# Kernel optimization log

Hardware: AMD Instinct MI355X
Metric: run time of the kernel (lower is better)

The kernel has to match this reference:

```python
import jax, jax.numpy as jnp
import numpy as np

N_CELLS = 6
N_OPS = 5
HIDDEN = 1024
IN_DIM = 376
OUT_DIM = 17
MAX_OUTPUT = 1.0
TAU = 1.0
BATCH = 2048

# op order matches the torch module: Tanh, ReLU, ELU, LeakyReLU(0.01), NullOp
ACTS = [jnp.tanh, jax.nn.relu, jax.nn.elu,
        lambda v: jax.nn.leaky_relu(v, 0.01),
        lambda v: jnp.zeros_like(v)]


def _apply_ops(pre):
    # pre: [j, o, b, h] -> apply the o-th activation to the o-th slice
    return jnp.stack([ACTS[o](pre[:, o]) for o in range(N_OPS)], axis=1)


def setup_inputs() -> dict:
    key = jax.random.key(0)
    ks = jax.random.split(key, 8)
    bw0 = 1.0 / np.sqrt(IN_DIM)
    bwh = 1.0 / np.sqrt(HIDDEN)
    x = jax.random.normal(ks[0], (BATCH, IN_DIM), dtype=jnp.float32)
    # stacked edge weights: W0 for cell-0 edges (input_dim -> hidden),
    # Wh[i-1] for cell-i edges (hidden -> hidden), i = 1..n_cells-2
    W0 = jax.random.uniform(ks[1], (N_CELLS, N_OPS, IN_DIM, HIDDEN), minval=-bw0, maxval=bw0, dtype=jnp.float32)
    b0 = jax.random.uniform(ks[2], (N_CELLS, N_OPS, HIDDEN), minval=-bw0, maxval=bw0, dtype=jnp.float32)
    Wh = jax.random.uniform(ks[3], (N_CELLS - 2, N_CELLS, N_OPS, HIDDEN, HIDDEN), minval=-bwh, maxval=bwh, dtype=jnp.float32)
    bh = jax.random.uniform(ks[4], (N_CELLS - 2, N_CELLS, N_OPS, HIDDEN), minval=-bwh, maxval=bwh, dtype=jnp.float32)
    Wout = jax.random.uniform(ks[5], (HIDDEN, OUT_DIM), minval=-bwh, maxval=bwh, dtype=jnp.float32)
    bout = jax.random.uniform(ks[6], (OUT_DIM,), minval=-bwh, maxval=bwh, dtype=jnp.float32)
    log_alphas = jnp.full((N_CELLS - 1, N_CELLS, N_OPS), -np.log(N_OPS), dtype=jnp.float32)
    # Gumbel noise (the torch module draws this in self.sample())
    u = jax.random.uniform(ks[7], (N_CELLS - 1, N_CELLS, N_OPS), minval=1e-6, maxval=1.0 - 1e-6, dtype=jnp.float32)
    eps = -jnp.log(-jnp.log(u))
    return {"x": x, "W0": W0, "b0": b0, "Wh": Wh, "bh": bh,
            "Wout": Wout, "bout": bout, "log_alphas": log_alphas, "eps": eps}


def reference(x, W0, b0, Wh, bh, Wout, bout, log_alphas, eps):
    # Gumbel-softmax mixing weights over the op axis
    z = jax.nn.softmax((log_alphas + eps) / TAU, axis=-1)  # [n_cells-1, n_cells, n_ops]
    # cell 0 feeds every node j >= 1: one batched GEMM over (j, o)
    pre0 = jnp.einsum('bd,jodh->jobh', x, W0[1:]) + b0[1:, :, None, :]
    outs = [(1, _apply_ops(pre0))]  # (first absolute j index, [j, o, b, h])
    tmp = None
    for i in range(1, N_CELLS):
        # node i input: weighted sum over all incoming edges k < i and ops o
        acc = jnp.zeros((x.shape[0], HIDDEN), dtype=x.dtype)
        for k in range(i):
            start, arr = outs[k]
            acc = acc + jnp.einsum('o,obh->bh', z[k, i], arr[i - start])
        if i < N_CELLS - 1:
            # node i feeds nodes j > i: batched GEMM over (j, o)
            pre = jnp.einsum('bh,johg->jobg', acc, Wh[i - 1, i + 1:]) + bh[i - 1, i + 1:, :, None, :]
            outs.append((i + 1, _apply_ops(pre)))
        tmp = acc
    return MAX_OUTPUT * jnp.tanh(tmp @ Wout + bout)
```

## Files before the change

### kernel.cpp

```cpp
#include <hip/hip_runtime.h>
#include <hip/hip_fp16.h>

typedef unsigned short u16;
typedef _Float16 f16;
typedef __attribute__((ext_vector_type(4))) u16 u16x4;
typedef __attribute__((ext_vector_type(8))) f16 f16x8;
typedef __attribute__((ext_vector_type(4))) float f32x4;

#define BATCH   2048
#define IN_DIM  376
#define KPAD0   384
#define HIDDEN  1024
#define OUT_DIM 17

#define WS_Z     0
#define WS_X16   1024
#define WS_ACC16 (WS_X16 + (size_t)BATCH*KPAD0*2)
#define WS_ACCF  (WS_ACC16 + (size_t)4*BATCH*HIDDEN*2)
#define WS_W0T   (WS_ACCF + (size_t)5*BATCH*HIDDEN*4)
#define WS_WHT   (WS_W0T + (size_t)20*HIDDEN*KPAD0*2)

__device__ __constant__ int D_PREF[5] = {0, 0, 4, 7, 9};

__device__ inline void gll16(const void* g, void* l) {
    __builtin_amdgcn_global_load_lds(
        (const __attribute__((address_space(1))) unsigned int*)g,
        (__attribute__((address_space(3))) unsigned int*)l, 16, 0, 0);
}

__global__ void z_kernel(const float* __restrict__ la, const float* __restrict__ ep,
                         float* __restrict__ z) {
    int t = threadIdx.x;
    if (t >= 30) return;
    float v[5]; float mx = -1e30f;
    #pragma unroll
    for (int o = 0; o < 5; ++o) { v[o] = la[t*5+o] + ep[t*5+o]; mx = fmaxf(mx, v[o]); }
    float s = 0.f;
    #pragma unroll
    for (int o = 0; o < 5; ++o) { v[o] = expf(v[o] - mx); s += v[o]; }
    float inv = 1.f / s;
    #pragma unroll
    for (int o = 0; o < 5; ++o) z[t*5+o] = v[o] * inv;
}

__global__ void xcvt_kernel(const float* __restrict__ x, u16* __restrict__ x16) {
    int idx = blockIdx.x * 256 + threadIdx.x;
    int b = idx / KPAD0, c = idx % KPAD0;
    float v = (c < IN_DIM) ? x[(size_t)b*IN_DIM + c] : 0.f;
    f16 h = (f16)v;
    x16[idx] = __builtin_bit_cast(u16, h);
}

__global__ void wtrans0_kernel(const float* __restrict__ W0, u16* __restrict__ dst) {
    __shared__ u16 sT[64*68];
    int bid = blockIdx.x;
    int mat = bid / 96, rem = bid % 96;
    int kt = rem / 16, nt = rem % 16;
    int i = mat / 4 + 1, o = mat % 4;
    const float* src = W0 + (size_t)(i*5 + o) * IN_DIM * HIDDEN;
    int t = threadIdx.x;
    #pragma unroll
    for (int p = 0; p < 16; ++p) {
        int e = p*256 + t;
        int kr = e >> 6, nc = e & 63;
        int k = kt*64 + kr;
        float v = (k < IN_DIM) ? src[(size_t)k*HIDDEN + nt*64 + nc] : 0.f;
        f16 h = (f16)v;
        sT[nc*68 + kr] = __builtin_bit_cast(u16, h);
    }
    __syncthreads();
    u16* d = dst + (size_t)mat * HIDDEN * KPAD0;
    #pragma unroll
    for (int p = 0; p < 4; ++p) {
        int c = p*256 + t;
        int nc = c >> 4, k4 = (c & 15) * 4;
        u16x4 v;
        #pragma unroll
        for (int j = 0; j < 4; ++j) v[j] = sT[nc*68 + k4 + j];
        *(u16x4*)&d[(size_t)(nt*64 + nc)*KPAD0 + kt*64 + k4] = v;
    }
}

__global__ void wtransH_kernel(const float* __restrict__ Wh, u16* __restrict__ dst) {
    const int SK[10] = {1,1,1,1,2,2,2,3,3,4};
    const int SI[10] = {2,3,4,5,3,4,5,4,5,5};
    __shared__ u16 sT[64*68];
    int bid = blockIdx.x;
    int mat = bid >> 8, rem = bid & 255;
    int kt = rem / 16, nt = rem % 16;
    int e = mat / 4, o = mat % 4;
    const float* src = Wh + (size_t)(((SK[e]-1)*6 + SI[e])*5 + o) * HIDDEN * HIDDEN;
    int t = threadIdx.x;
    #pragma unroll
    for (int p = 0; p < 16; ++p) {
        int ee = p*256 + t;
        int kr = ee >> 6, nc = ee & 63;
        float v = src[(size_t)(kt*64 + kr)*HIDDEN + nt*64 + nc];
        f16 h = (f16)v;
        sT[nc*68 + kr] = __builtin_bit_cast(u16, h);
    }
    __syncthreads();
    u16* d = dst + (size_t)mat * HIDDEN * HIDDEN;
    #pragma unroll
    for (int p = 0; p < 4; ++p) {
        int c = p*256 + t;
        int nc = c >> 4, k4 = (c & 15) * 4;
        u16x4 v;
        #pragma unroll
        for (int j = 0; j < 4; ++j) v[j] = sT[nc*68 + k4 + j];
        *(u16x4*)&d[(size_t)(nt*64 + nc)*HIDDEN + kt*64 + k4] = v;
    }
}

__global__ void zero_kernel(float* __restrict__ p) {
    int idx = blockIdx.x * 256 + threadIdx.x;
    *(f32x4*)&p[(size_t)idx*4] = (f32x4){0.f, 0.f, 0.f, 0.f};
}

__global__ void cvt_kernel(const float* __restrict__ src, u16* __restrict__ dst) {
    int idx = blockIdx.x * 256 + threadIdx.x;
    f32x4 v = *(const f32x4*)&src[(size_t)idx*4];
    u16x4 h;
    #pragma unroll
    for (int j = 0; j < 4; ++j) { f16 x = (f16)v[j]; h[j] = __builtin_bit_cast(u16, x); }
    *(u16x4*)&dst[(size_t)idx*4] = h;
}

__global__ __launch_bounds__(256)
void step_kernel(int stepi,
                 const u16* __restrict__ x16, const u16* __restrict__ acc16,
                 float* __restrict__ accf,
                 const u16* __restrict__ w0t, const u16* __restrict__ wht,
                 const float* __restrict__ b0, const float* __restrict__ bh,
                 const float* __restrict__ zws) {
    __shared__ alignas(16) u16 sA[64*64];
    __shared__ alignas(16) u16 sB[4][64*64];
    const int t = threadIdx.x;
    const int lane = t & 63, wid = t >> 6;
    const int l15 = lane & 15, lk = lane >> 4;

    const int bid  = blockIdx.x;
    const int slot = bid & 7;
    const int q    = bid >> 3;
    const int m0   = (q & 31) * 64;
    const int e    = (q >> 5) * 8 + slot;
    const int k    = e >> 4;
    const int n0   = (e & 15) * 64;

    const u16* Ap; int ldA, nks;
    const u16* Wt; int ldW;
    const float* bias;
    if (k == 0) {
        Ap = x16; ldA = KPAD0; nks = KPAD0/64;
        Wt = w0t + (size_t)((stepi-1)*4) * HIDDEN * KPAD0; ldW = KPAD0;
        bias = b0 + (size_t)(stepi*5) * HIDDEN;
    } else {
        Ap = acc16 + (size_t)(k-1) * BATCH * HIDDEN; ldA = HIDDEN; nks = HIDDEN/64;
        int eidx = D_PREF[k] + (stepi - k - 1);
        Wt = wht + (size_t)(eidx*4) * HIDDEN * HIDDEN; ldW = HIDDEN;
        bias = bh + (size_t)(((k-1)*6 + stepi)*5) * HIDDEN;
    }
    const float* zp = zws + (k*6 + stepi)*5;

    const int srow = lane >> 3;
    const int sc   = (lane & 7) ^ srow;

    const u16* aG0 = Ap + (size_t)(m0 + wid*16 + srow)     * ldA + sc*8;
    const u16* aG1 = Ap + (size_t)(m0 + wid*16 + 8 + srow) * ldA + sc*8;
    u16* aL0 = &sA[(wid*2)   * 512];
    u16* aL1 = &sA[(wid*2+1) * 512];
    const u16* Wop = Wt + (size_t)wid * HIDDEN * ldW;
    const u16* bG[8];
    #pragma unroll
    for (int p = 0; p < 8; ++p)
        bG[p] = Wop + (size_t)(n0 + p*8 + srow) * ldW + sc*8;
    u16* bL = &sB[wid][0];

    f32x4 acc[4][4] = {};

    for (int kb = 0; kb < nks; ++kb) {
        const int koff = kb * 64;
        gll16(aG0 + koff, aL0);
        gll16(aG1 + koff, aL1);
        #pragma unroll
        for (int p = 0; p < 8; ++p)
            gll16(bG[p] + koff, bL + p*512);
        __syncthreads();
        #pragma unroll
        for (int kc = 0; kc < 2; ++kc) {
            f16x8 af[4], bf[4];
            #pragma unroll
            for (int f = 0; f < 4; ++f) {
                int row = f*16 + l15;
                int cc = (kc*4 + lk) ^ (row & 7);
                af[f] = *(const f16x8*)&sA[row*64 + cc*8];
            }
            #pragma unroll
            for (int o = 0; o < 4; ++o) {
                int row = wid*16 + l15;
                int cc = (kc*4 + lk) ^ (row & 7);
                bf[o] = *(const f16x8*)&sB[o][row*64 + cc*8];
            }
            #pragma unroll
            for (int o = 0; o < 4; ++o)
                #pragma unroll
                for (int f = 0; f < 4; ++f)
                    acc[f][o] = __builtin_amdgcn_mfma_f32_16x16x32_f16(af[f], bf[o], acc[f][o], 0, 0, 0);
        }
        __syncthreads();
    }

    const int colw = n0 + wid*16 + l15;
    float outv[4][4] = {};
    #pragma unroll
    for (int o = 0; o < 4; ++o) {
        float zv = zp[o];
        float bv = bias[(size_t)o*HIDDEN + colw];
        #pragma unroll
        for (int f = 0; f < 4; ++f)
            #pragma unroll
            for (int r = 0; r < 4; ++r) {
                float pre = acc[f][o][r] + bv;
                float a;
                if      (o == 0) a = tanhf(pre);
                else if (o == 1) a = fmaxf(pre, 0.f);
                else if (o == 2) a = (pre > 0.f) ? pre : expm1f(pre);
                else             a = (pre > 0.f) ? pre : 0.01f * pre;
                outv[f][r] += zv * a;
            }
    }
    #pragma unroll
    for (int f = 0; f < 4; ++f)
        #pragma unroll
        for (int r = 0; r < 4; ++r)
            atomicAdd(&accf[(size_t)(m0 + f*16 + lk*4 + r)*HIDDEN + colw], outv[f][r]);
}

__global__ void out_kernel(const float* __restrict__ acc5, const float* __restrict__ Wout,
                           const float* __restrict__ bout, float* __restrict__ out) {
    int t = threadIdx.x;
    int g = t & 15, rl = t >> 4;
    int row = blockIdx.x * 16 + rl;
    const float* a = acc5 + (size_t)row * HIDDEN;
    float s[OUT_DIM] = {};
    for (int kk = 0; kk < HIDDEN/16; ++kk) {
        int kidx = kk*16 + g;
        float av = a[kidx];
        const float* wr = Wout + (size_t)kidx * OUT_DIM;
        #pragma unroll
        for (int j = 0; j < OUT_DIM; ++j) s[j] += av * wr[j];
    }
    #pragma unroll
    for (int m = 1; m < 16; m <<= 1) {
        #pragma unroll
        for (int j = 0; j < OUT_DIM; ++j) s[j] += __shfl_xor(s[j], m, 64);
    }
    if (g == 0) {
        #pragma unroll
        for (int j = 0; j < OUT_DIM; ++j)
            out[(size_t)row*OUT_DIM + j] = tanhf(s[j] + bout[j]);
    }
}

extern "C" void kernel_launch(void* const* d_in, const int* in_sizes, int n_in,
                              void* d_out, int out_size, void* d_ws, size_t ws_size,
                              hipStream_t stream) {
    const float* x    = (const float*)d_in[0];
    const float* W0   = (const float*)d_in[1];
    const float* b0   = (const float*)d_in[2];
    const float* Wh   = (const float*)d_in[3];
    const float* bh   = (const float*)d_in[4];
    const float* Wout = (const float*)d_in[5];
    const float* bout = (const float*)d_in[6];
    const float* la   = (const float*)d_in[7];
    const float* eps  = (const float*)d_in[8];
    float* out = (float*)d_out;

    char* ws = (char*)d_ws;
    float* zws  = (float*)(ws + WS_Z);
    u16* x16    = (u16*)(ws + WS_X16);
    u16* acc16  = (u16*)(ws + WS_ACC16);
    float* accf = (float*)(ws + WS_ACCF);
    u16* w0t    = (u16*)(ws + WS_W0T);
    u16* wht    = (u16*)(ws + WS_WHT);

    z_kernel<<<1, 32, 0, stream>>>(la, eps, zws);
    xcvt_kernel<<<(BATCH*KPAD0)/256, 256, 0, stream>>>(x, x16);
    wtrans0_kernel<<<1920, 256, 0, stream>>>(W0, w0t);
    wtransH_kernel<<<10240, 256, 0, stream>>>(Wh, wht);
    zero_kernel<<<(5*BATCH*HIDDEN)/(4*256), 256, 0, stream>>>(accf);

    for (int i = 1; i <= 5; ++i) {
        float* accf_i = accf + (size_t)(i-1)*BATCH*HIDDEN;
        step_kernel<<<512*i, 256, 0, stream>>>(
            i, x16, acc16, accf_i, w0t, wht, b0, bh, zws);
        if (i < 5)
            cvt_kernel<<<(BATCH*HIDDEN)/(4*256), 256, 0, stream>>>(
                accf_i, acc16 + (size_t)(i-1)*BATCH*HIDDEN);
    }
    out_kernel<<<BATCH/16, 256, 0, stream>>>(accf + (size_t)4*BATCH*HIDDEN, Wout, bout, out);
}
```

Before: 1.038 ms.

## Loop over incoming edges inside step kernel, drop atomics and convert passes

Each step kernel now runs 512 blocks, and each block iterates over all incoming edges k, accumulating the mixed activations in registers. This replaces the split-k grid that combined partial results with float atomics. The block writes fp16 output directly, or fp32 for the last step, so the zero and convert kernels go away. The two weight-transpose kernels are merged into one launch, and the LDS is double-buffered so the next tile loads while the current one computes. The trade-off is fewer blocks per launch and a serial K loop per block, which may reduce parallelism at the later steps.

```diff
diff --git a/kernel.cpp b/kernel.cpp
--- a/kernel.cpp
+++ b/kernel.cpp
@@ -51,90 +51,75 @@
     x16[idx] = __builtin_bit_cast(u16, h);
 }
 
-__global__ void wtrans0_kernel(const float* __restrict__ W0, u16* __restrict__ dst) {
+__global__ void wtrans_kernel(const float* __restrict__ W0, const float* __restrict__ Wh,
+                              u16* __restrict__ dst0, u16* __restrict__ dstH) {
     __shared__ u16 sT[64*68];
     int bid = blockIdx.x;
-    int mat = bid / 96, rem = bid % 96;
-    int kt = rem / 16, nt = rem % 16;
-    int i = mat / 4 + 1, o = mat % 4;
-    const float* src = W0 + (size_t)(i*5 + o) * IN_DIM * HIDDEN;
     int t = threadIdx.x;
-    #pragma unroll
-    for (int p = 0; p < 16; ++p) {
-        int e = p*256 + t;
-        int kr = e >> 6, nc = e & 63;
-        int k = kt*64 + kr;
-        float v = (k < IN_DIM) ? src[(size_t)k*HIDDEN + nt*64 + nc] : 0.f;
-        f16 h = (f16)v;
-        sT[nc*68 + kr] = __builtin_bit_cast(u16, h);
-    }
-    __syncthreads();
-    u16* d = dst + (size_t)mat * HIDDEN * KPAD0;
-    #pragma unroll
-    for (int p = 0; p < 4; ++p) {
-        int c = p*256 + t;
-        int nc = c >> 4, k4 = (c & 15) * 4;
-        u16x4 v;
-        #pragma unroll
-        for (int j = 0; j < 4; ++j) v[j] = sT[nc*68 + k4 + j];
-        *(u16x4*)&d[(size_t)(nt*64 + nc)*KPAD0 + kt*64 + k4] = v;
-    }
-}
-
-__global__ void wtransH_kernel(const float* __restrict__ Wh, u16* __restrict__ dst) {
-    const int SK[10] = {1,1,1,1,2,2,2,3,3,4};
-    const int SI[10] = {2,3,4,5,3,4,5,4,5,5};
-    __shared__ u16 sT[64*68];
-    int bid = blockIdx.x;
-    int mat = bid >> 8, rem = bid & 255;
-    int kt = rem / 16, nt = rem % 16;
-    int e = mat / 4, o = mat % 4;
-    const float* src = Wh + (size_t)(((SK[e]-1)*6 + SI[e])*5 + o) * HIDDEN * HIDDEN;
-    int t = threadIdx.x;
-    #pragma unroll
-    for (int p = 0; p < 16; ++p) {
-        int ee = p*256 + t;
-        int kr = ee >> 6, nc = ee & 63;
-        float v = src[(size_t)(kt*64 + kr)*HIDDEN + nt*64 + nc];
-        f16 h = (f16)v;
-        sT[nc*68 + kr] = __builtin_bit_cast(u16, h);
-    }
-    __syncthreads();
-    u16* d = dst + (size_t)mat * HIDDEN * HIDDEN;
-    #pragma unroll
-    for (int p = 0; p < 4; ++p) {
-        int c = p*256 + t;
-        int nc = c >> 4, k4 = (c & 15) * 4;
-        u16x4 v;
-        #pragma unroll
-        for (int j = 0; j < 4; ++j) v[j] = sT[nc*68 + k4 + j];
-        *(u16x4*)&d[(size_t)(nt*64 + nc)*HIDDEN + kt*64 + k4] = v;
-    }
-}
-
-__global__ void zero_kernel(float* __restrict__ p) {
-    int idx = blockIdx.x * 256 + threadIdx.x;
-    *(f32x4*)&p[(size_t)idx*4] = (f32x4){0.f, 0.f, 0.f, 0.f};
-}
-
-__global__ void cvt_kernel(const float* __restrict__ src, u16* __restrict__ dst) {
-    int idx = blockIdx.x * 256 + threadIdx.x;
-    f32x4 v = *(const f32x4*)&src[(size_t)idx*4];
-    u16x4 h;
-    #pragma unroll
-    for (int j = 0; j < 4; ++j) { f16 x = (f16)v[j]; h[j] = __builtin_bit_cast(u16, x); }
-    *(u16x4*)&dst[(size_t)idx*4] = h;
+    if (bid < 1920) {
+        int mat = bid / 96, rem = bid % 96;
+        int kt = rem / 16, nt = rem % 16;
+        int i = mat / 4 + 1, o = mat % 4;
+        const float* src = W0 + (size_t)(i*5 + o) * IN_DIM * HIDDEN;
+        #pragma unroll
+        for (int p = 0; p < 16; ++p) {
+            int e = p*256 + t;
+            int kr = e >> 6, nc = e & 63;
+            int k = kt*64 + kr;
+            float v = (k < IN_DIM) ? src[(size_t)k*HIDDEN + nt*64 + nc] : 0.f;
+            f16 h = (f16)v;
+            sT[nc*68 + kr] = __builtin_bit_cast(u16, h);
+        }
+        __syncthreads();
+        u16* d = dst0 + (size_t)mat * HIDDEN * KPAD0;
+        #pragma unroll
+        for (int p = 0; p < 4; ++p) {
+            int c = p*256 + t;
+            int nc = c >> 4, k4 = (c & 15) * 4;
+            u16x4 v;
+            #pragma unroll
+            for (int j = 0; j < 4; ++j) v[j] = sT[nc*68 + k4 + j];
+            *(u16x4*)&d[(size_t)(nt*64 + nc)*KPAD0 + kt*64 + k4] = v;
+        }
+    } else {
+        const int SK[10] = {1,1,1,1,2,2,2,3,3,4};
+        const int SI[10] = {2,3,4,5,3,4,5,4,5,5};
+        int bid2 = bid - 1920;
+        int mat = bid2 >> 8, rem = bid2 & 255;
+        int kt = rem / 16, nt = rem % 16;
+        int e = mat / 4, o = mat % 4;
+        const float* src = Wh + (size_t)(((SK[e]-1)*6 + SI[e])*5 + o) * HIDDEN * HIDDEN;
+        #pragma unroll
+        for (int p = 0; p < 16; ++p) {
+            int ee = p*256 + t;
+            int kr = ee >> 6, nc = ee & 63;
+            float v = src[(size_t)(kt*64 + kr)*HIDDEN + nt*64 + nc];
+            f16 h = (f16)v;
+            sT[nc*68 + kr] = __builtin_bit_cast(u16, h);
+        }
+        __syncthreads();
+        u16* d = dstH + (size_t)mat * HIDDEN * HIDDEN;
+        #pragma unroll
+        for (int p = 0; p < 4; ++p) {
+            int c = p*256 + t;
+            int nc = c >> 4, k4 = (c & 15) * 4;
+            u16x4 v;
+            #pragma unroll
+            for (int j = 0; j < 4; ++j) v[j] = sT[nc*68 + k4 + j];
+            *(u16x4*)&d[(size_t)(nt*64 + nc)*HIDDEN + kt*64 + k4] = v;
+        }
+    }
 }
 
 __global__ __launch_bounds__(256)
 void step_kernel(int stepi,
                  const u16* __restrict__ x16, const u16* __restrict__ acc16,
-                 float* __restrict__ accf,
+                 u16* __restrict__ acc16out, float* __restrict__ accf5,
                  const u16* __restrict__ w0t, const u16* __restrict__ wht,
                  const float* __restrict__ b0, const float* __restrict__ bh,
                  const float* __restrict__ zws) {
-    __shared__ alignas(16) u16 sA[64*64];
-    __shared__ alignas(16) u16 sB[4][64*64];
+    __shared__ alignas(16) u16 sA[2][64*64];
+    __shared__ alignas(16) u16 sB[2][4][64*64];
     const int t = threadIdx.x;
     const int lane = t & 63, wid = t >> 6;
     const int l15 = lane & 15, lk = lane >> 4;
@@ -143,97 +128,120 @@
     const int slot = bid & 7;
     const int q    = bid >> 3;
     const int m0   = (q & 31) * 64;
-    const int e    = (q >> 5) * 8 + slot;
-    const int k    = e >> 4;
-    const int n0   = (e & 15) * 64;
-
-    const u16* Ap; int ldA, nks;
-    const u16* Wt; int ldW;
-    const float* bias;
-    if (k == 0) {
-        Ap = x16; ldA = KPAD0; nks = KPAD0/64;
-        Wt = w0t + (size_t)((stepi-1)*4) * HIDDEN * KPAD0; ldW = KPAD0;
-        bias = b0 + (size_t)(stepi*5) * HIDDEN;
-    } else {
-        Ap = acc16 + (size_t)(k-1) * BATCH * HIDDEN; ldA = HIDDEN; nks = HIDDEN/64;
-        int eidx = D_PREF[k] + (stepi - k - 1);
-        Wt = wht + (size_t)(eidx*4) * HIDDEN * HIDDEN; ldW = HIDDEN;
-        bias = bh + (size_t)(((k-1)*6 + stepi)*5) * HIDDEN;
-    }
-    const float* zp = zws + (k*6 + stepi)*5;
+    const int n0   = ((q >> 5) * 8 + slot) * 64;
 
     const int srow = lane >> 3;
     const int sc   = (lane & 7) ^ srow;
 
-    const u16* aG0 = Ap + (size_t)(m0 + wid*16 + srow)     * ldA + sc*8;
-    const u16* aG1 = Ap + (size_t)(m0 + wid*16 + 8 + srow) * ldA + sc*8;
-    u16* aL0 = &sA[(wid*2)   * 512];
-    u16* aL1 = &sA[(wid*2+1) * 512];
-    const u16* Wop = Wt + (size_t)wid * HIDDEN * ldW;
-    const u16* bG[8];
-    #pragma unroll
-    for (int p = 0; p < 8; ++p)
-        bG[p] = Wop + (size_t)(n0 + p*8 + srow) * ldW + sc*8;
-    u16* bL = &sB[wid][0];
+    const u16* aG0; const u16* aG1; const u16* bG[8]; int snks;
+    auto setup = [&](int k) {
+        const u16* Ap; int ldA; const u16* Wt; int ldW;
+        if (k == 0) {
+            Ap = x16; ldA = KPAD0; snks = KPAD0/64;
+            Wt = w0t + (size_t)((stepi-1)*4) * HIDDEN * KPAD0; ldW = KPAD0;
+        } else {
+            Ap = acc16 + (size_t)(k-1) * BATCH * HIDDEN; ldA = HIDDEN; snks = HIDDEN/64;
+            int eidx = D_PREF[k] + (stepi - k - 1);
+            Wt = wht + (size_t)(eidx*4) * HIDDEN * HIDDEN; ldW = HIDDEN;
+        }
+        aG0 = Ap + (size_t)(m0 + wid*16 + srow)     * ldA + sc*8;
+        aG1 = Ap + (size_t)(m0 + wid*16 + 8 + srow) * ldA + sc*8;
+        const u16* Wop = Wt + (size_t)wid * HIDDEN * ldW;
+        #pragma unroll
+        for (int p = 0; p < 8; ++p)
+            bG[p] = Wop + (size_t)(n0 + p*8 + srow) * ldW + sc*8;
+    };
+    auto stage = [&](int buf, int kb) {
+        const int koff = kb * 64;
+        gll16(aG0 + koff, &sA[buf][(wid*2)   * 512]);
+        gll16(aG1 + koff, &sA[buf][(wid*2+1) * 512]);
+        #pragma unroll
+        for (int p = 0; p < 8; ++p)
+            gll16(bG[p] + koff, &sB[buf][wid][p*512]);
+    };
 
     f32x4 acc[4][4] = {};
-
-    for (int kb = 0; kb < nks; ++kb) {
-        const int koff = kb * 64;
-        gll16(aG0 + koff, aL0);
-        gll16(aG1 + koff, aL1);
-        #pragma unroll
-        for (int p = 0; p < 8; ++p)
-            gll16(bG[p] + koff, bL + p*512);
-        __syncthreads();
-        #pragma unroll
-        for (int kc = 0; kc < 2; ++kc) {
-            f16x8 af[4], bf[4];
-            #pragma unroll
-            for (int f = 0; f < 4; ++f) {
-                int row = f*16 + l15;
-                int cc = (kc*4 + lk) ^ (row & 7);
-                af[f] = *(const f16x8*)&sA[row*64 + cc*8];
+    float outv[4][4] = {};
+    const int colw = n0 + wid*16 + l15;
+
+    setup(0);
+    stage(0, 0);
+    int sk = 0, skb = 1;
+    int cur = 0;
+    __syncthreads();
+
+    for (int ck = 0; ck < stepi; ++ck) {
+        const int nk = (ck == 0) ? (KPAD0/64) : (HIDDEN/64);
+        for (int kb = 0; kb < nk; ++kb) {
+            if (skb == snks) { sk++; skb = 0; if (sk < stepi) setup(sk); }
+            if (sk < stepi) { stage(cur ^ 1, skb); skb++; }
+
+            #pragma unroll
+            for (int kc = 0; kc < 2; ++kc) {
+                f16x8 af[4], bf[4];
+                #pragma unroll
+                for (int f = 0; f < 4; ++f) {
+                    int row = f*16 + l15;
+                    int cc = (kc*4 + lk) ^ (row & 7);
+                    af[f] = *(const f16x8*)&sA[cur][row*64 + cc*8];
+                }
+                #pragma unroll
+                for (int o = 0; o < 4; ++o) {
+                    int row = wid*16 + l15;
+                    int cc = (kc*4 + lk) ^ (row & 7);
+                    bf[o] = *(const f16x8*)&sB[cur][o][row*64 + cc*8];
+                }
+                #pragma unroll
+                for (int o = 0; o < 4; ++o)
+                    #pragma unroll
+                    for (int f = 0; f < 4; ++f)
+                        acc[f][o] = __builtin_amdgcn_mfma_f32_16x16x32_f16(af[f], bf[o], acc[f][o], 0, 0, 0);
             }
-            #pragma unroll
-            for (int o = 0; o < 4; ++o) {
-                int row = wid*16 + l15;
-                int cc = (kc*4 + lk) ^ (row & 7);
-                bf[o] = *(const f16x8*)&sB[o][row*64 + cc*8];
+
+            if (kb == nk - 1) {
+                const float* zp   = zws + (ck*6 + stepi)*5;
+                const float* bias = (ck == 0)
+                    ? b0 + (size_t)(stepi*5) * HIDDEN
+                    : bh + (size_t)(((ck-1)*6 + stepi)*5) * HIDDEN;
+                #pragma unroll
+                for (int o = 0; o < 4; ++o) {
+                    float zv = zp[o];
+                    float bv = bias[(size_t)o*HIDDEN + colw];
+                    #pragma unroll
+                    for (int f = 0; f < 4; ++f)
+                        #pragma unroll
+                        for (int r = 0; r < 4; ++r) {
+                            float pre = acc[f][o][r] + bv;
+                            float a;
+                            if      (o == 0) a = tanhf(pre);
+                            else if (o == 1) a = fmaxf(pre, 0.f);
+                            else if (o == 2) a = (pre > 0.f) ? pre : expm1f(pre);
+                            else             a = (pre > 0.f) ? pre : 0.01f * pre;
+                            outv[f][r] += zv * a;
+                            acc[f][o][r] = 0.f;
+                        }
+                }
             }
-            #pragma unroll
-            for (int o = 0; o < 4; ++o)
-                #pragma unroll
-                for (int f = 0; f < 4; ++f)
-                    acc[f][o] = __builtin_amdgcn_mfma_f32_16x16x32_f16(af[f], bf[o], acc[f][o], 0, 0, 0);
-        }
-        __syncthreads();
-    }
-
-    const int colw = n0 + wid*16 + l15;
-    float outv[4][4] = {};
-    #pragma unroll
-    for (int o = 0; o < 4; ++o) {
-        float zv = zp[o];
-        float bv = bias[(size_t)o*HIDDEN + colw];
+            __syncthreads();
+            cur ^= 1;
+        }
+    }
+
+    if (stepi < 5) {
         #pragma unroll
         for (int f = 0; f < 4; ++f)
             #pragma unroll
             for (int r = 0; r < 4; ++r) {
-                float pre = acc[f][o][r] + bv;
-                float a;
-                if      (o == 0) a = tanhf(pre);
-                else if (o == 1) a = fmaxf(pre, 0.f);
-                else if (o == 2) a = (pre > 0.f) ? pre : expm1f(pre);
-                else             a = (pre > 0.f) ? pre : 0.01f * pre;
-                outv[f][r] += zv * a;
+                f16 h = (f16)outv[f][r];
+                acc16out[(size_t)(m0 + f*16 + lk*4 + r)*HIDDEN + colw] = __builtin_bit_cast(u16, h);
             }
-    }
-    #pragma unroll
-    for (int f = 0; f < 4; ++f)
-        #pragma unroll
-        for (int r = 0; r < 4; ++r)
-            atomicAdd(&accf[(size_t)(m0 + f*16 + lk*4 + r)*HIDDEN + colw], outv[f][r]);
+    } else {
+        #pragma unroll
+        for (int f = 0; f < 4; ++f)
+            #pragma unroll
+            for (int r = 0; r < 4; ++r)
+                accf5[(size_t)(m0 + f*16 + lk*4 + r)*HIDDEN + colw] = outv[f][r];
+    }
 }
 
 __global__ void out_kernel(const float* __restrict__ acc5, const float* __restrict__ Wout,
@@ -286,17 +294,12 @@
 
     z_kernel<<<1, 32, 0, stream>>>(la, eps, zws);
     xcvt_kernel<<<(BATCH*KPAD0)/256, 256, 0, stream>>>(x, x16);
-    wtrans0_kernel<<<1920, 256, 0, stream>>>(W0, w0t);
-    wtransH_kernel<<<10240, 256, 0, stream>>>(Wh, wht);
-    zero_kernel<<<(5*BATCH*HIDDEN)/(4*256), 256, 0, stream>>>(accf);
+    wtrans_kernel<<<1920 + 10240, 256, 0, stream>>>(W0, Wh, w0t, wht);
 
     for (int i = 1; i <= 5; ++i) {
-        float* accf_i = accf + (size_t)(i-1)*BATCH*HIDDEN;
-        step_kernel<<<512*i, 256, 0, stream>>>(
-            i, x16, acc16, accf_i, w0t, wht, b0, bh, zws);
-        if (i < 5)
-            cvt_kernel<<<(BATCH*HIDDEN)/(4*256), 256, 0, stream>>>(
-                accf_i, acc16 + (size_t)(i-1)*BATCH*HIDDEN);
-    }
-    out_kernel<<<BATCH/16, 256, 0, stream>>>(accf + (size_t)4*BATCH*HIDDEN, Wout, bout, out);
-}
+        u16* a16o = acc16 + (size_t)(i-1)*BATCH*HIDDEN;
+        step_kernel<<<512, 256, 0, stream>>>(
+            i, x16, acc16, a16o, accf, w0t, wht, b0, bh, zws);
+    }
+    out_kernel<<<BATCH/16, 256, 0, stream>>>(accf, Wout, bout, out);
+}
```

Result: slower. 1.215 ms (+17.1%).
